# Kernel optimization log

Hardware: AMD Instinct MI355X
Metric: run time of the kernel (lower is better)

The kernel has to match this reference:

```python
import jax, jax.numpy as jnp
import numpy as np

N_NODES = 19385
N_EDGES = 1_200_000
GNN = 256
HID = 512
RANK = 512
NCLS = 3
NGENES = 6640
NBLK = 6
B = 256
EPS = 1e-5


def _ln(x, g, b):
    m = jnp.mean(x, axis=-1, keepdims=True)
    v = jnp.mean(jnp.square(x - m), axis=-1, keepdims=True)
    return (x - m) * jax.lax.rsqrt(v + EPS) * g + b


def setup_inputs() -> dict:
    key = jax.random.key(0)
    ks = iter(jax.random.split(key, 40))
    w = lambda shape, s=0.02: jax.random.normal(next(ks), shape, jnp.float32) * s
    inp = {
        'node_idx': jax.random.randint(next(ks), (B,), -1, N_NODES),  # -1 == OOV
        'edge_index': jax.random.randint(next(ks), (2, N_EDGES), 0, N_NODES),
        'edge_weight': jax.random.uniform(next(ks), (N_EDGES,), jnp.float32),
        'frozen_emb': jax.random.normal(next(ks), (N_NODES, GNN), jnp.float32),
        # trainable partial GNN (mps.6, mps.7, post_mp)
        'conv6_W': w((GNN, GNN)), 'conv6_b': jnp.zeros((GNN,)),
        'ln6_g': jnp.ones((GNN,)), 'ln6_b': jnp.zeros((GNN,)),
        'conv7_W': w((GNN, GNN)), 'conv7_b': jnp.zeros((GNN,)),
        'ln7_g': jnp.ones((GNN,)), 'ln7_b': jnp.zeros((GNN,)),
        'post_W': w((GNN, GNN)), 'post_b': jnp.zeros((GNN,)),
        # head
        'oov_emb': w((GNN,)),
        'in_ln_g': jnp.ones((GNN,)), 'in_ln_b': jnp.zeros((GNN,)),
        'proj_in_W': w((GNN, HID)), 'proj_in_b': jnp.zeros((HID,)),
        'rb_ln_g': jnp.ones((NBLK, HID)), 'rb_ln_b': jnp.zeros((NBLK, HID)),
        'rb_W1': w((NBLK, HID, 4 * HID)), 'rb_b1': jnp.zeros((NBLK, 4 * HID)),
        'rb_W2': w((NBLK, 4 * HID, HID)), 'rb_b2': jnp.zeros((NBLK, HID)),
        'out_ln_g': jnp.ones((HID,)), 'out_ln_b': jnp.zeros((HID,)),
        'bil_W': w((HID, NCLS * RANK)), 'bil_b': jnp.zeros((NCLS * RANK,)),
        'out_gene_emb': w((NGENES, RANK)),
    }
    return inp


def reference(node_idx, edge_index, edge_weight, frozen_emb,
              conv6_W, conv6_b, ln6_g, ln6_b,
              conv7_W, conv7_b, ln7_g, ln7_b,
              post_W, post_b,
              oov_emb, in_ln_g, in_ln_b, proj_in_W, proj_in_b,
              rb_ln_g, rb_ln_b, rb_W1, rb_b1, rb_W2, rb_b2,
              out_ln_g, out_ln_b, bil_W, bil_b, out_gene_emb):
    src, dst = edge_index[0], edge_index[1]

    def conv(x, W, b):
        # edge-weighted message passing: gather -> scale -> scatter-add -> linear
        msg = x[src] * edge_weight[:, None]              # [E, GNN]
        agg = jax.ops.segment_sum(msg, dst, num_segments=N_NODES)
        return agg @ W + b

    # trainable GNN layers (eval mode: dropout = identity)
    x = frozen_emb
    x = x + jax.nn.relu(_ln(conv(x, conv6_W, conv6_b), ln6_g, ln6_b))
    x = x + jax.nn.relu(_ln(conv(x, conv7_W, conv7_b), ln7_g, ln7_b))
    node_emb = x @ post_W + post_b                       # [N, GNN]

    # OOV-aware lookup
    in_f = (node_idx >= 0).astype(jnp.float32)[:, None]  # [B,1]
    gnn_emb = node_emb[jnp.clip(node_idx, 0, None)]      # [B, GNN]
    h = gnn_emb * in_f + oov_emb[None, :] * (1.0 - in_f)

    # MLP head
    h = _ln(h, in_ln_g, in_ln_b) @ proj_in_W + proj_in_b
    for i in range(NBLK):
        t = _ln(h, rb_ln_g[i], rb_ln_b[i])
        t = jax.nn.gelu(t @ rb_W1[i] + rb_b1[i])
        h = h + t @ rb_W2[i] + rb_b2[i]
    h = _ln(h, out_ln_g, out_ln_b)

    pert = (h @ bil_W + bil_b).reshape(B, NCLS, RANK)
    logits = jnp.einsum('bcr,gr->bcg', pert, out_gene_emb)  # [B, 3, 6640]
    return logits
```

## Files before the change

### kernel.cpp

```cpp
#include <hip/hip_runtime.h>
#include <hip/hip_bf16.h>
#include <cstdint>
#include <cstddef>

#define N_NODES_C 19385
#define N_EDGES_C 1200000
#define GNN_C 256
#define HID_C 512
#define RANK_C 512
#define NCLS_C 3
#define NGENES_C 6640
#define NBLK_C 6
#define B_C 256
#define LN_EPS 1e-5f

#define PH_K 128
#define PH_CHUNK (N_EDGES_C / PH_K)
#define PH_NW ((N_NODES_C + 1) / 2)

typedef short bf8v __attribute__((ext_vector_type(8)));
typedef float f4v __attribute__((ext_vector_type(4)));
typedef int i2v __attribute__((ext_vector_type(2)));

__device__ __forceinline__ float bfu2f(unsigned short u) {
  union { unsigned int i; float f; } c; c.i = ((unsigned)u) << 16; return c.f;
}
__device__ __forceinline__ unsigned short f2bfu(float v) {
  union { float f; unsigned u; } c; c.f = v;
  unsigned r = c.u + 0x7FFFu + ((c.u >> 16) & 1u);
  return (unsigned short)(r >> 16);
}
__device__ __forceinline__ float gelu_tanh(float v) {
  const float x3 = v * v * v;
  return 0.5f * v * (1.f + tanhf(0.7978845608028654f * (v + 0.044715f * x3)));
}


struct CvtSeg { const float* s; unsigned short* d; long long n; };
struct CvtArgs { CvtSeg seg[2]; int nseg; };

__global__ __launch_bounds__(256) void multicvt_kernel(CvtArgs a) {
  for (int sg = 0; sg < a.nseg; ++sg) {
    const float4* s = reinterpret_cast<const float4*>(a.seg[sg].s);
    unsigned short* d = a.seg[sg].d;
    const long long n4 = a.seg[sg].n >> 2;
    for (long long i = blockIdx.x * 256 + threadIdx.x; i < n4;
         i += (long long)gridDim.x * 256) {
      float4 v = s[i];
      ushort4 o;
      o.x = f2bfu(v.x); o.y = f2bfu(v.y); o.z = f2bfu(v.z); o.w = f2bfu(v.w);
      *reinterpret_cast<ushort4*>(d + i * 4) = o;
    }
  }
}


struct TSeg { const float* s; unsigned short* d; int R, C; };
struct TArgs { TSeg seg[12]; int nseg; };

__global__ __launch_bounds__(256) void multitrans_kernel(TArgs a) {
  __shared__ float tile[32][33];
  const int tx = threadIdx.x & 31;
  const int ty = threadIdx.x >> 5;
  for (int sg = 0; sg < a.nseg; ++sg) {
    const int R = a.seg[sg].R, C = a.seg[sg].C;
    const int tC = C >> 5;
    const int nt = (R >> 5) * tC;
    const float* src = a.seg[sg].s;
    unsigned short* dst = a.seg[sg].d;
    for (int tid = blockIdx.x; tid < nt; tid += gridDim.x) {
      const int tr = tid / tC, tc = tid - tr * tC;
      const int r0 = tr * 32, c0 = tc * 32;
      __syncthreads();
#pragma unroll
      for (int j = 0; j < 32; j += 8)
        tile[ty + j][tx] = src[(size_t)(r0 + ty + j) * C + c0 + tx];
      __syncthreads();
#pragma unroll
      for (int j = 0; j < 32; j += 8)
        dst[(size_t)(c0 + ty + j) * R + r0 + tx] = f2bfu(tile[tx][ty + j]);
    }
  }
}


__global__ __launch_bounds__(256) void marksel_kernel(const int* __restrict__ node_idx,
                                                      int* __restrict__ selbm,
                                                      int* __restrict__ needed) {
  const int b = threadIdx.x;
  const int n = max(node_idx[b], 0);
  selbm[n] = 1;
  needed[n] = 1;
}

__global__ __launch_bounds__(256) void privhist_kernel(const int* __restrict__ src,
                                                       const int* __restrict__ dst,
                                                       const int* __restrict__ selbm,
                                                       int* __restrict__ needed,
                                                       unsigned int* __restrict__ cntp) {
  __shared__ unsigned int bins[PH_NW];
  const int t = threadIdx.x;
  for (int w = t; w < PH_NW; w += 256) bins[w] = 0u;
  __syncthreads();
  const int base = blockIdx.x * PH_CHUNK;
  const int end = base + PH_CHUNK;
#pragma unroll 4
  for (int i = base + t; i < end; i += 256) {
    const int d = dst[i];
    atomicAdd(&bins[d >> 1], 1u << ((d & 1) * 16));
    if (selbm[d]) needed[src[i]] = 1;
  }
  __syncthreads();
  unsigned int* out = cntp + (size_t)blockIdx.x * PH_NW;
  for (int w = t; w < PH_NW; w += 256) out[w] = bins[w];
}

__global__ __launch_bounds__(256) void redhist_kernel(const unsigned int* __restrict__ cntp,
                                                      int* __restrict__ cnt) {
  const int w = blockIdx.x * 256 + threadIdx.x;
  if (w >= PH_NW) return;
  unsigned int lo = 0, hi = 0;
#pragma unroll 4
  for (int k = 0; k < PH_K; ++k) {
    const unsigned int u = cntp[(size_t)k * PH_NW + w];
    lo += u & 0xFFFFu;
    hi += u >> 16;
  }
  cnt[2 * w] = (int)lo;
  if (2 * w + 1 < N_NODES_C) cnt[2 * w + 1] = (int)hi;
}

__global__ __launch_bounds__(1024) void scan_kernel(const int* __restrict__ cnt,
                                                    int* __restrict__ off, int n) {
  __shared__ int sums[1024];
  const int t = threadIdx.x;
  const int CH = (n + 1023) >> 10;
  const int base = t * CH;
  int s = 0;
  for (int i = 0; i < CH; ++i) {
    int idx = base + i;
    if (idx < n) s += cnt[idx];
  }
  sums[t] = s;
  __syncthreads();
  for (int d = 1; d < 1024; d <<= 1) {
    int v = (t >= d) ? sums[t - d] : 0;
    __syncthreads();
    sums[t] += v;
    __syncthreads();
  }
  int run = (t == 0) ? 0 : sums[t - 1];
  for (int i = 0; i < CH; ++i) {
    int idx = base + i;
    if (idx < n) { off[idx] = run; run += cnt[idx]; }
  }
  if (t == 0) off[n] = sums[1023];
}

__global__ __launch_bounds__(256) void fill_kernel(const int* __restrict__ src,
                                                   const int* __restrict__ dst,
                                                   const float* __restrict__ ew,
                                                   const int* __restrict__ off,
                                                   int* __restrict__ cur,
                                                   const int* __restrict__ needed,
                                                   i2v* __restrict__ ep, int E) {
  const int i = blockIdx.x * 256 + threadIdx.x;
  if (i < E) {
    const int d = dst[i];
    if (needed[d]) {
      const int p = atomicAdd(&cur[d], 1);
      i2v e;
      e[0] = src[i] * GNN_C;
      e[1] = __float_as_int(ew[i]);
      ep[off[d] + p] = e;
    }
  }
}


__global__ __launch_bounds__(256) void agg_full_kernel(const i2v* __restrict__ ep,
                                                       const int* __restrict__ off,
                                                       const int* __restrict__ needed,
                                                       const unsigned short* __restrict__ x,
                                                       unsigned short* __restrict__ aggbf) {
  const int n = blockIdx.x;
  if (!needed[n]) return;
  __shared__ f4v red[4][64];
  const int t = threadIdx.x;
  const int w = __builtin_amdgcn_readfirstlane(t >> 6);
  const int lane = t & 63;
  const int s0 = off[n];
  const int c = off[n + 1] - s0;
  const int q0 = s0 + ((c * w) >> 2);
  const int q1 = s0 + ((c * (w + 1)) >> 2);
  float a0 = 0.f, a1 = 0.f, a2 = 0.f, a3 = 0.f;
  const unsigned short* xl = x + 4 * lane;
#pragma unroll 4
  for (int p = q0; p < q1; ++p) {
    const i2v e = ep[p];
    const int s = e[0];
    const float wg = __int_as_float(e[1]);
    const ushort4 v = *reinterpret_cast<const ushort4*>(xl + s);
    a0 = fmaf(bfu2f(v.x), wg, a0);
    a1 = fmaf(bfu2f(v.y), wg, a1);
    a2 = fmaf(bfu2f(v.z), wg, a2);
    a3 = fmaf(bfu2f(v.w), wg, a3);
  }
  f4v av; av[0] = a0; av[1] = a1; av[2] = a2; av[3] = a3;
  red[w][lane] = av;
  __syncthreads();
  const float* rf = reinterpret_cast<const float*>(red);
  const float sum = rf[t] + rf[256 + t] + rf[512 + t] + rf[768 + t];
  aggbf[(size_t)n * GNN_C + t] = f2bfu(sum);
}

__global__ __launch_bounds__(256) void agg_sel_kernel(const int* __restrict__ node_idx,
                                                      const i2v* __restrict__ ep,
                                                      const int* __restrict__ off,
                                                      const float* __restrict__ x,
                                                      unsigned short* __restrict__ aggbf) {
  __shared__ f4v red[4][64];
  const int b = blockIdx.x;
  const int t = threadIdx.x;
  const int n = max(node_idx[b], 0);
  const int w = __builtin_amdgcn_readfirstlane(t >> 6);
  const int lane = t & 63;
  const int s0 = off[n];
  const int c = off[n + 1] - s0;
  const int q0 = s0 + ((c * w) >> 2);
  const int q1 = s0 + ((c * (w + 1)) >> 2);
  float a0 = 0.f, a1 = 0.f, a2 = 0.f, a3 = 0.f;
  const float* xl = x + 4 * lane;
#pragma unroll 2
  for (int p = q0; p < q1; ++p) {
    const i2v e = ep[p];
    const int s = e[0];
    const float wg = __int_as_float(e[1]);
    const f4v v = *reinterpret_cast<const f4v*>(xl + s);
    a0 = fmaf(v[0], wg, a0);
    a1 = fmaf(v[1], wg, a1);
    a2 = fmaf(v[2], wg, a2);
    a3 = fmaf(v[3], wg, a3);
  }
  f4v av; av[0] = a0; av[1] = a1; av[2] = a2; av[3] = a3;
  red[w][lane] = av;
  __syncthreads();
  const float* rf = reinterpret_cast<const float*>(red);
  const float sum = rf[t] + rf[256 + t] + rf[512 + t] + rf[768 + t];
  aggbf[(size_t)b * GNN_C + t] = f2bfu(sum);
}


#define MBK 32
#define MLDW 40

__global__ __launch_bounds__(256) void mgemm_kernel(const unsigned short* __restrict__ A,
                                                    const unsigned short* __restrict__ Bt,
                                                    const float* __restrict__ bias,
                                                    float* __restrict__ C,
                                                    int M, int N, int K) {
  __shared__ unsigned short As[128][MLDW];
  __shared__ unsigned short Bs[128][MLDW];
  const int t = threadIdx.x;
  const int lane = t & 63;
  const int wave = t >> 6;
  const int r0 = blockIdx.x * 128;
  const int c0 = blockIdx.y * 128;
  const int wm = (wave >> 1) * 64;
  const int wn = (wave & 1) * 64;
  const int lm = lane & 15;
  const int lq = lane >> 4;

  f4v acc[4][4];
  for (int i = 0; i < 4; ++i)
    for (int j = 0; j < 4; ++j)
      for (int r = 0; r < 4; ++r) acc[i][j][r] = 0.f;

  const int row = t >> 1;
  const int kof = (t & 1) * 16;
  for (int k0 = 0; k0 < K; k0 += MBK) {
    {
      const int gr = r0 + row;
      uint4 u0 = make_uint4(0, 0, 0, 0), u1 = u0;
      if (gr < M) {
        const uint4* p = reinterpret_cast<const uint4*>(A + (size_t)gr * K + k0 + kof);
        u0 = p[0]; u1 = p[1];
      }
      *reinterpret_cast<uint4*>(&As[row][kof]) = u0;
      *reinterpret_cast<uint4*>(&As[row][kof + 8]) = u1;
    }
    {
      const int gn = c0 + row;
      uint4 u0 = make_uint4(0, 0, 0, 0), u1 = u0;
      if (gn < N) {
        const uint4* p = reinterpret_cast<const uint4*>(Bt + (size_t)gn * K + k0 + kof);
        u0 = p[0]; u1 = p[1];
      }
      *reinterpret_cast<uint4*>(&Bs[row][kof]) = u0;
      *reinterpret_cast<uint4*>(&Bs[row][kof + 8]) = u1;
    }
    __syncthreads();

    bf8v a[4], b[4];
#pragma unroll
    for (int i = 0; i < 4; ++i)
      a[i] = *reinterpret_cast<const bf8v*>(&As[wm + i * 16 + lm][lq * 8]);
#pragma unroll
    for (int j = 0; j < 4; ++j)
      b[j] = *reinterpret_cast<const bf8v*>(&Bs[wn + j * 16 + lm][lq * 8]);
#pragma unroll
    for (int i = 0; i < 4; ++i)
#pragma unroll
      for (int j = 0; j < 4; ++j)
        acc[i][j] = __builtin_amdgcn_mfma_f32_16x16x32_bf16(a[i], b[j], acc[i][j], 0, 0, 0);
    __syncthreads();
  }

  for (int ti = 0; ti < 4; ++ti) {
    for (int tj = 0; tj < 4; ++tj) {
      const int col = c0 + wn + tj * 16 + lm;
      if (col >= N) continue;
      const float bv = bias ? bias[col] : 0.f;
      for (int r = 0; r < 4; ++r) {
        const int row2 = r0 + wm + ti * 16 + lq * 4 + r;
        if (row2 < M) C[(size_t)row2 * N + col] = acc[ti][tj][r] + bv;
      }
    }
  }
}


__global__ __launch_bounds__(256) void mgemm64_kernel(const unsigned short* __restrict__ A,
                                                      const unsigned short* __restrict__ Bt,
                                                      const float* __restrict__ bias,
                                                      float* outF, unsigned short* outB,
                                                      int M, int N, int K, int doGelu) {
  __shared__ unsigned short As[64][MLDW];
  __shared__ unsigned short Bs[64][MLDW];
  const int t = threadIdx.x;
  const int lane = t & 63;
  const int wave = t >> 6;
  const int r0 = blockIdx.x * 64;
  const int c0 = blockIdx.y * 64;
  const int wm = (wave >> 1) * 32;
  const int wn = (wave & 1) * 32;
  const int lm = lane & 15;
  const int lq = lane >> 4;

  f4v acc[2][2];
  for (int i = 0; i < 2; ++i)
    for (int j = 0; j < 2; ++j)
      for (int r = 0; r < 4; ++r) acc[i][j][r] = 0.f;

  const int row = t >> 2;
  const int kof = (t & 3) * 8;
  for (int k0 = 0; k0 < K; k0 += MBK) {
    *reinterpret_cast<uint4*>(&As[row][kof]) =
        *reinterpret_cast<const uint4*>(A + (size_t)(r0 + row) * K + k0 + kof);
    *reinterpret_cast<uint4*>(&Bs[row][kof]) =
        *reinterpret_cast<const uint4*>(Bt + (size_t)(c0 + row) * K + k0 + kof);
    __syncthreads();
    bf8v a[2], b[2];
#pragma unroll
    for (int i = 0; i < 2; ++i)
      a[i] = *reinterpret_cast<const bf8v*>(&As[wm + i * 16 + lm][lq * 8]);
#pragma unroll
    for (int j = 0; j < 2; ++j)
      b[j] = *reinterpret_cast<const bf8v*>(&Bs[wn + j * 16 + lm][lq * 8]);
#pragma unroll
    for (int i = 0; i < 2; ++i)
#pragma unroll
      for (int j = 0; j < 2; ++j)
        acc[i][j] = __builtin_amdgcn_mfma_f32_16x16x32_bf16(a[i], b[j], acc[i][j], 0, 0, 0);
    __syncthreads();
  }

  for (int ti = 0; ti < 2; ++ti) {
    for (int tj = 0; tj < 2; ++tj) {
      const int col = c0 + wn + tj * 16 + lm;
      const float bv = bias ? bias[col] : 0.f;
      for (int r = 0; r < 4; ++r) {
        const int row2 = r0 + wm + ti * 16 + lq * 4 + r;
        float v = acc[ti][tj][r] + bv;
        if (doGelu) v = gelu_tanh(v);
        if (outF) outF[(size_t)row2 * N + col] = v;
        else outB[(size_t)row2 * N + col] = f2bfu(v);
      }
    }
  }
}

__global__ __launch_bounds__(256) void skmgemm64_kernel(const unsigned short* __restrict__ A,
                                                        const unsigned short* __restrict__ Bt,
                                                        float* __restrict__ part,
                                                        int M, int N, int K, int kc) {
  __shared__ unsigned short As[64][MLDW];
  __shared__ unsigned short Bs[64][MLDW];
  const int t = threadIdx.x;
  const int lane = t & 63;
  const int wave = t >> 6;
  const int r0 = blockIdx.x * 64;
  const int c0 = blockIdx.y * 64;
  const int kBeg = blockIdx.z * kc;
  const int kEnd = kBeg + kc;
  const int wm = (wave >> 1) * 32;
  const int wn = (wave & 1) * 32;
  const int lm = lane & 15;
  const int lq = lane >> 4;

  f4v acc[2][2];
  for (int i = 0; i < 2; ++i)
    for (int j = 0; j < 2; ++j)
      for (int r = 0; r < 4; ++r) acc[i][j][r] = 0.f;

  const int row = t >> 2;
  const int kof = (t & 3) * 8;
  for (int k0 = kBeg; k0 < kEnd; k0 += MBK) {
    *reinterpret_cast<uint4*>(&As[row][kof]) =
        *reinterpret_cast<const uint4*>(A + (size_t)(r0 + row) * K + k0 + kof);
    *reinterpret_cast<uint4*>(&Bs[row][kof]) =
        *reinterpret_cast<const uint4*>(Bt + (size_t)(c0 + row) * K + k0 + kof);
    __syncthreads();
    bf8v a[2], b[2];
#pragma unroll
    for (int i = 0; i < 2; ++i)
      a[i] = *reinterpret_cast<const bf8v*>(&As[wm + i * 16 + lm][lq * 8]);
#pragma unroll
    for (int j = 0; j < 2; ++j)
      b[j] = *reinterpret_cast<const bf8v*>(&Bs[wn + j * 16 + lm][lq * 8]);
#pragma unroll
    for (int i = 0; i < 2; ++i)
#pragma unroll
      for (int j = 0; j < 2; ++j)
        acc[i][j] = __builtin_amdgcn_mfma_f32_16x16x32_bf16(a[i], b[j], acc[i][j], 0, 0, 0);
    __syncthreads();
  }

  float* out = part + (size_t)blockIdx.z * M * N;
  for (int ti = 0; ti < 2; ++ti)
    for (int tj = 0; tj < 2; ++tj) {
      const int col = c0 + wn + tj * 16 + lm;
      for (int r = 0; r < 4; ++r) {
        const int row2 = r0 + wm + ti * 16 + lq * 4 + r;
        out[(size_t)row2 * N + col] = acc[ti][tj][r];
      }
    }
}


__global__ __launch_bounds__(256) void postconv6_kernel(const float* __restrict__ g,
                                                        const float* __restrict__ b,
                                                        const float* __restrict__ frozen,
                                                        const int* __restrict__ needed,
                                                        float* __restrict__ yx) {
  __shared__ float sb[4];
  const int n = blockIdx.x, t = threadIdx.x;
  if (!needed[n]) return;
  const float v = yx[(size_t)n * GNN_C + t];
  float s = v;
  for (int o = 32; o; o >>= 1) s += __shfl_down(s, o, 64);
  if ((t & 63) == 0) sb[t >> 6] = s;
  __syncthreads();
  const float m = (sb[0] + sb[1] + sb[2] + sb[3]) * (1.f / GNN_C);
  __syncthreads();
  const float d = v - m;
  s = d * d;
  for (int o = 32; o; o >>= 1) s += __shfl_down(s, o, 64);
  if ((t & 63) == 0) sb[t >> 6] = s;
  __syncthreads();
  const float rs = rsqrtf((sb[0] + sb[1] + sb[2] + sb[3]) * (1.f / GNN_C) + LN_EPS);
  const float xn = d * rs * g[t] + b[t];
  yx[(size_t)n * GNN_C + t] = frozen[(size_t)n * GNN_C + t] + fmaxf(xn, 0.f);
}

__global__ __launch_bounds__(256) void postconv7_kernel(const float* __restrict__ y,
                                                        const float* __restrict__ g,
                                                        const float* __restrict__ b,
                                                        const int* __restrict__ idx,
                                                        const float* __restrict__ x1f,
                                                        unsigned short* __restrict__ out) {
  __shared__ float sb[4];
  const int bi = blockIdx.x, t = threadIdx.x;
  const int n = max(idx[bi], 0);
  const float v = y[(size_t)bi * GNN_C + t];
  float s = v;
  for (int o = 32; o; o >>= 1) s += __shfl_down(s, o, 64);
  if ((t & 63) == 0) sb[t >> 6] = s;
  __syncthreads();
  const float m = (sb[0] + sb[1] + sb[2] + sb[3]) * (1.f / GNN_C);
  __syncthreads();
  const float d = v - m;
  s = d * d;
  for (int o = 32; o; o >>= 1) s += __shfl_down(s, o, 64);
  if ((t & 63) == 0) sb[t >> 6] = s;
  __syncthreads();
  const float rs = rsqrtf((sb[0] + sb[1] + sb[2] + sb[3]) * (1.f / GNN_C) + LN_EPS);
  const float xn = d * rs * g[t] + b[t];
  out[(size_t)bi * GNN_C + t] = f2bfu(x1f[(size_t)n * GNN_C + t] + fmaxf(xn, 0.f));
}

__global__ __launch_bounds__(256) void h0ln_kernel(const float* __restrict__ ne,
                                                   const int* __restrict__ idx,
                                                   const float* __restrict__ oov,
                                                   const float* __restrict__ g,
                                                   const float* __restrict__ b,
                                                   unsigned short* __restrict__ out) {
  __shared__ float sb[4];
  const int bi = blockIdx.x, t = threadIdx.x;
  const float v = (idx[bi] >= 0) ? ne[(size_t)bi * GNN_C + t] : oov[t];
  float s = v;
  for (int o = 32; o; o >>= 1) s += __shfl_down(s, o, 64);
  if ((t & 63) == 0) sb[t >> 6] = s;
  __syncthreads();
  const float m = (sb[0] + sb[1] + sb[2] + sb[3]) * (1.f / GNN_C);
  __syncthreads();
  const float d = v - m;
  s = d * d;
  for (int o = 32; o; o >>= 1) s += __shfl_down(s, o, 64);
  if ((t & 63) == 0) sb[t >> 6] = s;
  __syncthreads();
  const float rs = rsqrtf((sb[0] + sb[1] + sb[2] + sb[3]) * (1.f / GNN_C) + LN_EPS);
  out[(size_t)bi * GNN_C + t] = f2bfu(d * rs * g[t] + b[t]);
}

__global__ __launch_bounds__(256) void lnbf_kernel(const float* __restrict__ in,
                                                   const float* __restrict__ g,
                                                   const float* __restrict__ b,
                                                   unsigned short* __restrict__ out) {
  __shared__ float sb[4];
  const int r = blockIdx.x, t = threadIdx.x;
  const float v0 = in[(size_t)r * HID_C + t];
  const float v1 = in[(size_t)r * HID_C + t + 256];
  float s = v0 + v1;
  for (int o = 32; o; o >>= 1) s += __shfl_down(s, o, 64);
  if ((t & 63) == 0) sb[t >> 6] = s;
  __syncthreads();
  const float m = (sb[0] + sb[1] + sb[2] + sb[3]) * (1.f / HID_C);
  __syncthreads();
  const float d0 = v0 - m, d1 = v1 - m;
  s = d0 * d0 + d1 * d1;
  for (int o = 32; o; o >>= 1) s += __shfl_down(s, o, 64);
  if ((t & 63) == 0) sb[t >> 6] = s;
  __syncthreads();
  const float rs = rsqrtf((sb[0] + sb[1] + sb[2] + sb[3]) * (1.f / HID_C) + LN_EPS);
  out[(size_t)r * HID_C + t] = f2bfu(d0 * rs * g[t] + b[t]);
  out[(size_t)r * HID_C + t + 256] = f2bfu(d1 * rs * g[t + 256] + b[t + 256]);
}

__global__ __launch_bounds__(256) void combln_kernel(const float* __restrict__ part,
                                                     float* __restrict__ h,
                                                     const float* __restrict__ b2,
                                                     const float* __restrict__ g,
                                                     const float* __restrict__ b,
                                                     unsigned short* __restrict__ out) {
  __shared__ float sb[4];
  const int r = blockIdx.x, t = threadIdx.x;
  const int MN = B_C * HID_C;
  const size_t o0 = (size_t)r * HID_C + t;
  const size_t o1 = o0 + 256;
  float v0 = h[o0] + b2[t] + part[o0] + part[MN + o0] + part[2 * MN + o0] + part[3 * MN + o0];
  float v1 = h[o1] + b2[t + 256] + part[o1] + part[MN + o1] + part[2 * MN + o1] + part[3 * MN + o1];
  h[o0] = v0;
  h[o1] = v1;
  float s = v0 + v1;
  for (int o = 32; o; o >>= 1) s += __shfl_down(s, o, 64);
  if ((t & 63) == 0) sb[t >> 6] = s;
  __syncthreads();
  const float m = (sb[0] + sb[1] + sb[2] + sb[3]) * (1.f / HID_C);
  __syncthreads();
  const float d0 = v0 - m, d1 = v1 - m;
  s = d0 * d0 + d1 * d1;
  for (int o = 32; o; o >>= 1) s += __shfl_down(s, o, 64);
  if ((t & 63) == 0) sb[t >> 6] = s;
  __syncthreads();
  const float rs = rsqrtf((sb[0] + sb[1] + sb[2] + sb[3]) * (1.f / HID_C) + LN_EPS);
  out[o0] = f2bfu(d0 * rs * g[t] + b[t]);
  out[o1] = f2bfu(d1 * rs * g[t + 256] + b[t + 256]);
}


extern "C" void kernel_launch(void* const* d_in, const int* in_sizes, int n_in,
                              void* d_out, int out_size, void* d_ws, size_t ws_size,
                              hipStream_t stream) {
  const int* node_idx = (const int*)d_in[0];
  const int* e_src = (const int*)d_in[1];
  const int* e_dst = e_src + N_EDGES_C;
  const float* ew = (const float*)d_in[2];
  const float* frozen = (const float*)d_in[3];
  const float* W6 = (const float*)d_in[4];
  const float* b6 = (const float*)d_in[5];
  const float* g6 = (const float*)d_in[6];
  const float* bl6 = (const float*)d_in[7];
  const float* W7 = (const float*)d_in[8];
  const float* b7 = (const float*)d_in[9];
  const float* g7 = (const float*)d_in[10];
  const float* bl7 = (const float*)d_in[11];
  const float* postW = (const float*)d_in[12];
  const float* postb = (const float*)d_in[13];
  const float* oov = (const float*)d_in[14];
  const float* ing = (const float*)d_in[15];
  const float* inb = (const float*)d_in[16];
  const float* projW = (const float*)d_in[17];
  const float* projb = (const float*)d_in[18];
  const float* rbg = (const float*)d_in[19];
  const float* rbb = (const float*)d_in[20];
  const float* rbW1 = (const float*)d_in[21];
  const float* rbb1 = (const float*)d_in[22];
  const float* rbW2 = (const float*)d_in[23];
  const float* rbb2 = (const float*)d_in[24];
  const float* outg = (const float*)d_in[25];
  const float* outb = (const float*)d_in[26];
  const float* bilW = (const float*)d_in[27];
  const float* bilb = (const float*)d_in[28];
  const float* gene = (const float*)d_in[29];
  (void)in_sizes; (void)n_in; (void)out_size; (void)ws_size;

  char* ws = (char*)d_ws;
  size_t o = 0;
  auto alloc = [&](size_t bytes) -> char* {
    char* p = ws + o;
    o += (bytes + 255) & ~(size_t)255;
    return p;
  };
  int* cnt = (int*)alloc((size_t)N_NODES_C * 4);
  int* off = (int*)alloc((size_t)(N_NODES_C + 1) * 4);
  int* cur = (int*)alloc((size_t)N_NODES_C * 4);
  int* needed = (int*)alloc((size_t)N_NODES_C * 4);
  int* selbm = (int*)alloc((size_t)N_NODES_C * 4);
  unsigned int* cntp = (unsigned int*)alloc((size_t)PH_K * PH_NW * 4);
  i2v* ep = (i2v*)alloc((size_t)N_EDGES_C * 8);
  unsigned short* frozbf = (unsigned short*)alloc((size_t)N_NODES_C * GNN_C * 2);
  char* aggregion = alloc((size_t)NBLK_C * HID_C * 4 * HID_C * 2);
  unsigned short* w6t = (unsigned short*)alloc((size_t)GNN_C * GNN_C * 2);
  unsigned short* w7t = (unsigned short*)alloc((size_t)GNN_C * GNN_C * 2);
  unsigned short* postWt = (unsigned short*)alloc((size_t)GNN_C * GNN_C * 2);
  unsigned short* projWt = (unsigned short*)alloc((size_t)HID_C * GNN_C * 2);
  unsigned short* bilWt = (unsigned short*)alloc((size_t)NCLS_C * RANK_C * HID_C * 2);
  float* yx = (float*)alloc((size_t)N_NODES_C * GNN_C * 4);
  unsigned short* rbW2t = (unsigned short*)alloc((size_t)NBLK_C * 4 * HID_C * HID_C * 2);
  float* part = (float*)alloc((size_t)4 * B_C * HID_C * 4);
  unsigned short* agg7bf = (unsigned short*)alloc((size_t)B_C * GNN_C * 2);
  float* y7b = (float*)alloc((size_t)B_C * GNN_C * 4);
  unsigned short* x2bf = (unsigned short*)alloc((size_t)B_C * GNN_C * 2);
  float* nemb = (float*)alloc((size_t)B_C * GNN_C * 4);
  unsigned short* h0lbf = (unsigned short*)alloc((size_t)B_C * GNN_C * 2);
  float* h = (float*)alloc((size_t)B_C * HID_C * 4);
  unsigned short* tbf = (unsigned short*)alloc((size_t)B_C * HID_C * 2);
  unsigned short* ubf = (unsigned short*)alloc((size_t)B_C * 4 * HID_C * 2);
  unsigned short* pertbf = (unsigned short*)alloc((size_t)B_C * NCLS_C * RANK_C * 2);

  unsigned short* agg6bf = (unsigned short*)aggregion;
  unsigned short* rbW1t = (unsigned short*)aggregion;
  unsigned short* genebf = frozbf;

  (void)hipMemsetAsync(cur, 0, (size_t)N_NODES_C * 4, stream);
  (void)hipMemsetAsync(needed, 0, (size_t)N_NODES_C * 4, stream);
  (void)hipMemsetAsync(selbm, 0, (size_t)N_NODES_C * 4, stream);
  const int egrid = (N_EDGES_C + 255) / 256;
  marksel_kernel<<<1, 256, 0, stream>>>(node_idx, selbm, needed);
  privhist_kernel<<<PH_K, 256, 0, stream>>>(e_src, e_dst, selbm, needed, cntp);
  redhist_kernel<<<(PH_NW + 255) / 256, 256, 0, stream>>>(cntp, cnt);
  scan_kernel<<<1, 1024, 0, stream>>>(cnt, off, N_NODES_C);
  fill_kernel<<<egrid, 256, 0, stream>>>(e_src, e_dst, ew, off, cur, needed, ep, N_EDGES_C);

  {
    CvtArgs a;
    a.seg[0] = {frozen, frozbf, (long long)N_NODES_C * GNN_C};
    a.nseg = 1;
    multicvt_kernel<<<512, 256, 0, stream>>>(a);
  }
  {
    TArgs a;
    a.seg[0] = {W6, w6t, GNN_C, GNN_C};
    a.seg[1] = {W7, w7t, GNN_C, GNN_C};
    a.seg[2] = {postW, postWt, GNN_C, GNN_C};
    a.seg[3] = {projW, projWt, GNN_C, HID_C};
    a.seg[4] = {bilW, bilWt, HID_C, NCLS_C * RANK_C};
    a.nseg = 5;
    multitrans_kernel<<<512, 256, 0, stream>>>(a);
  }

  agg_full_kernel<<<N_NODES_C, 256, 0, stream>>>(ep, off, needed, frozbf, agg6bf);
  {
    dim3 g((N_NODES_C + 127) / 128, GNN_C / 128);
    mgemm_kernel<<<g, 256, 0, stream>>>(agg6bf, w6t, b6, yx, N_NODES_C, GNN_C, GNN_C);
  }
  postconv6_kernel<<<N_NODES_C, 256, 0, stream>>>(g6, bl6, frozen, needed, yx);

  {
    TArgs a;
    for (int i = 0; i < NBLK_C; ++i) {
      a.seg[i] = {rbW1 + (size_t)i * HID_C * 4 * HID_C,
                  rbW1t + (size_t)i * HID_C * 4 * HID_C, HID_C, 4 * HID_C};
      a.seg[6 + i] = {rbW2 + (size_t)i * 4 * HID_C * HID_C,
                      rbW2t + (size_t)i * 4 * HID_C * HID_C, 4 * HID_C, HID_C};
    }
    a.nseg = 12;
    multitrans_kernel<<<2048, 256, 0, stream>>>(a);
  }
  {
    CvtArgs a;
    a.seg[0] = {gene, genebf, (long long)NGENES_C * RANK_C};
    a.nseg = 1;
    multicvt_kernel<<<512, 256, 0, stream>>>(a);
  }

  agg_sel_kernel<<<B_C, 256, 0, stream>>>(node_idx, ep, off, yx, agg7bf);
  {
    dim3 g(B_C / 64, GNN_C / 64);
    mgemm64_kernel<<<g, 256, 0, stream>>>(agg7bf, w7t, b7, y7b, nullptr,
                                          B_C, GNN_C, GNN_C, 0);
  }
  postconv7_kernel<<<B_C, 256, 0, stream>>>(y7b, g7, bl7, node_idx, yx, x2bf);

  {
    dim3 g(B_C / 64, GNN_C / 64);
    mgemm64_kernel<<<g, 256, 0, stream>>>(x2bf, postWt, postb, nemb, nullptr,
                                          B_C, GNN_C, GNN_C, 0);
  }
  h0ln_kernel<<<B_C, 256, 0, stream>>>(nemb, node_idx, oov, ing, inb, h0lbf);

  {
    dim3 g(B_C / 64, HID_C / 64);
    mgemm64_kernel<<<g, 256, 0, stream>>>(h0lbf, projWt, projb, h, nullptr,
                                          B_C, HID_C, GNN_C, 0);
  }
  lnbf_kernel<<<B_C, 256, 0, stream>>>(h, rbg, rbb, tbf);

  for (int i = 0; i < NBLK_C; ++i) {
    {
      dim3 g(B_C / 64, (4 * HID_C) / 64);
      mgemm64_kernel<<<g, 256, 0, stream>>>(tbf, rbW1t + (size_t)i * HID_C * 4 * HID_C,
                                            rbb1 + (size_t)i * 4 * HID_C, nullptr, ubf,
                                            B_C, 4 * HID_C, HID_C, 1);
    }
    {
      dim3 g(B_C / 64, HID_C / 64, 4);
      skmgemm64_kernel<<<g, 256, 0, stream>>>(ubf, rbW2t + (size_t)i * 4 * HID_C * HID_C,
                                              part, B_C, HID_C, 4 * HID_C, HID_C);
    }
    const float* gn = (i < NBLK_C - 1) ? rbg + (size_t)(i + 1) * HID_C : outg;
    const float* bn = (i < NBLK_C - 1) ? rbb + (size_t)(i + 1) * HID_C : outb;
    combln_kernel<<<B_C, 256, 0, stream>>>(part, h, rbb2 + (size_t)i * HID_C, gn, bn, tbf);
  }

  {
    dim3 g(B_C / 64, (NCLS_C * RANK_C) / 64);
    mgemm64_kernel<<<g, 256, 0, stream>>>(tbf, bilWt, bilb, nullptr, pertbf,
                                          B_C, NCLS_C * RANK_C, HID_C, 0);
  }

  {
    dim3 g((B_C * NCLS_C) / 128, (NGENES_C + 127) / 128);
    mgemm_kernel<<<g, 256, 0, stream>>>(pertbf, genebf, nullptr, (float*)d_out,
                                        B_C * NCLS_C, NGENES_C, RANK_C);
  }
}
```

Before: 620.7 us.

## Replace global atomic CSR fill with per-block privatized LDS prefix ranks

The reduction kernel now writes each partition's exclusive prefix back into the per-block histogram. The fill kernel reuses the privhist edge partition and loads those prefixes into LDS. Each edge then gets its slot from a shared-memory atomic instead of a global atomic on a per-node cursor, which removes the cursor buffer and its memset. The partition count also rises from 128 to 192 to restore parallelism, at the cost of extra write-back traffic in the reduction and far fewer blocks for the fill kernel.

```diff
diff --git a/kernel.cpp b/kernel.cpp
--- a/kernel.cpp
+++ b/kernel.cpp
@@ -14,7 +14,7 @@
 #define B_C 256
 #define LN_EPS 1e-5f
 
-#define PH_K 128
+#define PH_K 192
 #define PH_CHUNK (N_EDGES_C / PH_K)
 #define PH_NW ((N_NODES_C + 1) / 2)
 
@@ -115,14 +115,16 @@
   for (int w = t; w < PH_NW; w += 256) out[w] = bins[w];
 }
 
-__global__ __launch_bounds__(256) void redhist_kernel(const unsigned int* __restrict__ cntp,
+__global__ __launch_bounds__(256) void redhist_kernel(unsigned int* __restrict__ cntp,
                                                       int* __restrict__ cnt) {
   const int w = blockIdx.x * 256 + threadIdx.x;
   if (w >= PH_NW) return;
   unsigned int lo = 0, hi = 0;
 #pragma unroll 4
   for (int k = 0; k < PH_K; ++k) {
-    const unsigned int u = cntp[(size_t)k * PH_NW + w];
+    const size_t idx = (size_t)k * PH_NW + w;
+    const unsigned int u = cntp[idx];
+    cntp[idx] = lo | (hi << 16);
     lo += u & 0xFFFFu;
     hi += u >> 16;
   }
@@ -161,19 +163,27 @@
                                                    const int* __restrict__ dst,
                                                    const float* __restrict__ ew,
                                                    const int* __restrict__ off,
-                                                   int* __restrict__ cur,
+                                                   const unsigned int* __restrict__ cntp,
                                                    const int* __restrict__ needed,
-                                                   i2v* __restrict__ ep, int E) {
-  const int i = blockIdx.x * 256 + threadIdx.x;
-  if (i < E) {
+                                                   i2v* __restrict__ ep) {
+  __shared__ unsigned int bins[PH_NW];
+  const int t = threadIdx.x;
+  const unsigned int* myp = cntp + (size_t)blockIdx.x * PH_NW;
+  for (int w = t; w < PH_NW; w += 256) bins[w] = myp[w];
+  __syncthreads();
+  const int base = blockIdx.x * PH_CHUNK;
+  const int end = base + PH_CHUNK;
+#pragma unroll 2
+  for (int i = base + t; i < end; i += 256) {
     const int d = dst[i];
-    if (needed[d]) {
-      const int p = atomicAdd(&cur[d], 1);
-      i2v e;
-      e[0] = src[i] * GNN_C;
-      e[1] = __float_as_int(ew[i]);
-      ep[off[d] + p] = e;
-    }
+    if (!needed[d]) continue;
+    const int sh = (d & 1) * 16;
+    const unsigned int old = atomicAdd(&bins[d >> 1], 1u << sh);
+    const int rank = (int)((old >> sh) & 0xFFFFu);
+    i2v e;
+    e[0] = src[i] * GNN_C;
+    e[1] = __float_as_int(ew[i]);
+    ep[off[d] + rank] = e;
   }
 }
 
@@ -624,7 +634,6 @@
   };
   int* cnt = (int*)alloc((size_t)N_NODES_C * 4);
   int* off = (int*)alloc((size_t)(N_NODES_C + 1) * 4);
-  int* cur = (int*)alloc((size_t)N_NODES_C * 4);
   int* needed = (int*)alloc((size_t)N_NODES_C * 4);
   int* selbm = (int*)alloc((size_t)N_NODES_C * 4);
   unsigned int* cntp = (unsigned int*)alloc((size_t)PH_K * PH_NW * 4);
@@ -653,15 +662,13 @@
   unsigned short* rbW1t = (unsigned short*)aggregion;
   unsigned short* genebf = frozbf;
 
-  (void)hipMemsetAsync(cur, 0, (size_t)N_NODES_C * 4, stream);
   (void)hipMemsetAsync(needed, 0, (size_t)N_NODES_C * 4, stream);
   (void)hipMemsetAsync(selbm, 0, (size_t)N_NODES_C * 4, stream);
-  const int egrid = (N_EDGES_C + 255) / 256;
   marksel_kernel<<<1, 256, 0, stream>>>(node_idx, selbm, needed);
   privhist_kernel<<<PH_K, 256, 0, stream>>>(e_src, e_dst, selbm, needed, cntp);
   redhist_kernel<<<(PH_NW + 255) / 256, 256, 0, stream>>>(cntp, cnt);
   scan_kernel<<<1, 1024, 0, stream>>>(cnt, off, N_NODES_C);
-  fill_kernel<<<egrid, 256, 0, stream>>>(e_src, e_dst, ew, off, cur, needed, ep, N_EDGES_C);
+  fill_kernel<<<PH_K, 256, 0, stream>>>(e_src, e_dst, ew, off, cntp, needed, ep);
 
   {
     CvtArgs a;
```

New measurement: 608.9 us. No clear change (-1.9%).
